# Kernel tuning notes

Hardware: AMD Instinct MI355X
Metric: run time of the kernel (lower is better)

Reference implementation:

```python
import jax, jax.numpy as jnp
import numpy as np

ALPHA = 0.2   # LeakyReLU negative slope
NEG = -1e9    # mask value for non-edges


def setup_inputs() -> dict:
    key = jax.random.key(0)
    ks = jax.random.split(key, 8)
    N, Din, F, H, Dout = 4096, 512, 64, 8, 16
    adj = (jax.random.uniform(ks[0], (N, N)) < 0.01).astype(jnp.float32)
    adjacency = jnp.maximum(adj, jnp.eye(N, dtype=jnp.float32))
    X = jax.random.normal(ks[1], (N, Din), jnp.float32)
    s = lambda k, shape, fan: jax.random.normal(k, shape, jnp.float32) / np.float32(np.sqrt(fan))
    W = s(ks[2], (H, Din, F), Din)        # per-head projection, stacked
    a1 = s(ks[3], (H, F), F)              # attention vector, source half
    a2 = s(ks[4], (H, F), F)              # attention vector, target half
    Wo = s(ks[5], (H * F, Dout), H * F)   # output-layer projection
    ao1 = s(ks[6], (Dout,), Dout)
    ao2 = s(ks[7], (Dout,), Dout)
    return dict(adjacency=adjacency, X=X, W=W, a1=a1, a2=a2, Wo=Wo, ao1=ao1, ao2=ao2)


def reference(adjacency, X, W, a1, a2, Wo, ao1, ao2):
    # dropout is identity (eval mode / p=0)
    mask = adjacency > 0
    N = X.shape[0]
    # --- multi-head attention layers (concat=True -> ELU) ---
    Wh = jnp.einsum('nd,hdf->hnf', X, W)                      # [H, N, F]
    f1 = jnp.einsum('hnf,hf->hn', Wh, a1)                     # [H, N]
    f2 = jnp.einsum('hnf,hf->hn', Wh, a2)                     # [H, N]
    e = jax.nn.leaky_relu(f1[:, :, None] + f2[:, None, :], ALPHA)  # [H, N, N]
    att = jax.nn.softmax(jnp.where(mask[None], e, NEG), axis=-1)
    heads = jax.nn.elu(jnp.einsum('hnm,hmf->hnf', att, Wh))   # [H, N, F]
    cat = jnp.transpose(heads, (1, 0, 2)).reshape(N, -1)      # [N, H*F]
    # --- output attention layer (concat=False -> no ELU) ---
    Who = cat @ Wo                                            # [N, Dout]
    eo = jax.nn.leaky_relu((Who @ ao1)[:, None] + (Who @ ao2)[None, :], ALPHA)
    atto = jax.nn.softmax(jnp.where(mask, eo, NEG), axis=-1)  # [N, N]
    return atto @ Who                                         # [N, Dout]
```

## Files before the change

### kernel.cpp

```cpp
#include <hip/hip_runtime.h>
#include <hip/hip_bf16.h>

#define N_NODES 4096
#define DIN     512
#define FDIM    64
#define NHEADS  8
#define DOUT    16
#define MAXN    512

typedef __attribute__((ext_vector_type(8))) short bf16x8;
typedef __attribute__((ext_vector_type(4))) float f32x4;

static __device__ __forceinline__ float us2f(unsigned short u) {
    union { unsigned int i; float f; } cv; cv.i = ((unsigned int)u) << 16; return cv.f;
}
static __device__ __forceinline__ unsigned short f2us(float v) {
    __hip_bfloat16 b = __float2bfloat16(v);
    return *(const unsigned short*)&b;
}

__global__ void detect_kernel(const unsigned short* __restrict__ adj, int* __restrict__ flag)
{
    if (threadIdx.x == 0) *flag = (adj[0] == 0) ? 1 : 0;
}

__global__ __launch_bounds__(256) void build_nbr_kernel(
    const void* __restrict__ adj, const int* __restrict__ flag,
    int* __restrict__ cnt, int* __restrict__ nbr)
{
    const int n = blockIdx.x;
    const int f32 = *flag;
    __shared__ int c;
    if (threadIdx.x == 0) c = 0;
    __syncthreads();
    if (f32) {
        const unsigned int* row = (const unsigned int*)adj + (size_t)n * N_NODES;
        for (int m = threadIdx.x; m < N_NODES; m += 256) {
            if (row[m]) { int p = atomicAdd(&c, 1); if (p < MAXN) nbr[(size_t)n * MAXN + p] = m; }
        }
    } else {
        const unsigned short* row = (const unsigned short*)adj + (size_t)n * N_NODES;
        for (int m = threadIdx.x; m < N_NODES; m += 256) {
            if (row[m]) { int p = atomicAdd(&c, 1); if (p < MAXN) nbr[(size_t)n * MAXN + p] = m; }
        }
    }
    __syncthreads();
    if (threadIdx.x == 0) cnt[n] = (c < MAXN) ? c : MAXN;
}

__global__ __launch_bounds__(256) void conv_small_kernel(
    const void* __restrict__ a1, const void* __restrict__ a2, const void* __restrict__ Wo,
    const void* __restrict__ ao1, const void* __restrict__ ao2,
    const int* __restrict__ flag, float* __restrict__ dst)
{
    const int f32 = *flag;
    const void* srcs[5] = { a1, a2, Wo, ao1, ao2 };
    const int   szs[5]  = { 512, 512, 8192, 16, 16 };
    int base = 0;
    for (int s = 0; s < 5; ++s) {
        if (f32) {
            for (int i = threadIdx.x; i < szs[s]; i += 256)
                dst[base + i] = ((const float*)srcs[s])[i];
        } else {
            for (int i = threadIdx.x; i < szs[s]; i += 256)
                dst[base + i] = us2f(((const unsigned short*)srcs[s])[i]);
        }
        base += szs[s];
    }
}

__global__ __launch_bounds__(256) void wh_mfma_kernel(
    const void* __restrict__ X, const void* __restrict__ W,
    const int* __restrict__ flag, unsigned short* __restrict__ Whb)
{
    __shared__ unsigned short Ah[64][72];
    __shared__ unsigned short Al[64][72];
    __shared__ unsigned short Bt[64][72];
    const int f32 = *flag;
    const int h  = blockIdx.x;
    const int bm = blockIdx.y;
    const int tid  = threadIdx.x;
    const int w    = tid >> 6;
    const int lane = tid & 63;
    const int quad = lane >> 4;
    const int l16  = lane & 15;
    const int r  = tid >> 2;
    const int c4 = (tid & 3) * 16;

    f32x4 acc[4];
#pragma unroll
    for (int j = 0; j < 4; ++j) acc[j] = (f32x4){0.f, 0.f, 0.f, 0.f};

    for (int k0 = 0; k0 < DIN; k0 += 64) {
        if (f32) {
            const float* xp = (const float*)X + (size_t)(bm * 64 + r) * DIN + k0 + c4;
            const float* wp = (const float*)W + (size_t)h * DIN * FDIM + (size_t)(k0 + r) * FDIM + c4;
#pragma unroll
            for (int i = 0; i < 16; ++i) {
                float v = xp[i];
                unsigned short hi = f2us(v);
                Ah[r][c4 + i] = hi;
                Al[r][c4 + i] = f2us(v - us2f(hi));
            }
#pragma unroll
            for (int i = 0; i < 16; ++i) Bt[c4 + i][r] = f2us(wp[i]);
        } else {
            const unsigned short* xp = (const unsigned short*)X + (size_t)(bm * 64 + r) * DIN + k0 + c4;
            const unsigned short* wp = (const unsigned short*)W + (size_t)h * DIN * FDIM + (size_t)(k0 + r) * FDIM + c4;
#pragma unroll
            for (int i = 0; i < 16; ++i) { Ah[r][c4 + i] = xp[i]; Al[r][c4 + i] = 0; }
#pragma unroll
            for (int i = 0; i < 16; ++i) Bt[c4 + i][r] = wp[i];
        }
        __syncthreads();
#pragma unroll
        for (int kk = 0; kk < 64; kk += 32) {
            bf16x8 a_hi = *(const bf16x8*)&Ah[w * 16 + l16][kk + quad * 8];
            bf16x8 a_lo = *(const bf16x8*)&Al[w * 16 + l16][kk + quad * 8];
#pragma unroll
            for (int j = 0; j < 4; ++j) {
                bf16x8 b = *(const bf16x8*)&Bt[j * 16 + l16][kk + quad * 8];
                acc[j] = __builtin_amdgcn_mfma_f32_16x16x32_bf16(a_hi, b, acc[j], 0, 0, 0);
                acc[j] = __builtin_amdgcn_mfma_f32_16x16x32_bf16(a_lo, b, acc[j], 0, 0, 0);
            }
        }
        __syncthreads();
    }
#pragma unroll
    for (int j = 0; j < 4; ++j) {
        int col = j * 16 + l16;
#pragma unroll
        for (int rr = 0; rr < 4; ++rr) {
            int row = bm * 64 + w * 16 + quad * 4 + rr;
            Whb[((size_t)h * N_NODES + row) * FDIM + col] = f2us(acc[j][rr]);
        }
    }
}

__global__ __launch_bounds__(256) void f12_kernel(
    const unsigned short* __restrict__ Whb,
    const float* __restrict__ a1c, const float* __restrict__ a2c,
    float* __restrict__ f1, float* __restrict__ f2)
{
    int idx = blockIdx.x * 256 + threadIdx.x;
    int h = idx >> 12;
    const unsigned short* row = Whb + (size_t)idx * FDIM;
    float s1 = 0.f, s2 = 0.f;
#pragma unroll
    for (int f = 0; f < FDIM; ++f) {
        float v = us2f(row[f]);
        s1 += v * a1c[h * FDIM + f];
        s2 += v * a2c[h * FDIM + f];
    }
    f1[idx] = s1;
    f2[idx] = s2;
}

__global__ __launch_bounds__(256) void attn1_kernel(
    const unsigned short* __restrict__ Whb,
    const float* __restrict__ f1, const float* __restrict__ f2,
    const int* __restrict__ cnt, const int* __restrict__ nbr,
    unsigned short* __restrict__ catb)
{
    const int n = blockIdx.x;
    const int tid = threadIdx.x;
    const int wid = tid >> 6;
    const int lane = tid & 63;
    __shared__ int sh_m[MAXN];
    __shared__ float sh_s[4][MAXN];
    const int c0 = cnt[n];
    const int c = (c0 < MAXN) ? c0 : MAXN;
    for (int k = tid; k < c; k += 256) sh_m[k] = nbr[(size_t)n * MAXN + k];
    __syncthreads();
    for (int hh = 0; hh < 2; ++hh) {
        const int h = wid * 2 + hh;
        const float f1v = f1[h * N_NODES + n];
        float mx = -1e30f;
        for (int k = lane; k < c; k += 64) {
            float s = f1v + f2[h * N_NODES + sh_m[k]];
            s = (s >= 0.f) ? s : 0.2f * s;
            sh_s[wid][k] = s;
            mx = fmaxf(mx, s);
        }
#pragma unroll
        for (int off = 32; off; off >>= 1) mx = fmaxf(mx, __shfl_xor(mx, off));
        float sum = 0.f;
        for (int k = lane; k < c; k += 64) {
            float e = __expf(sh_s[wid][k] - mx);
            sh_s[wid][k] = e;
            sum += e;
        }
#pragma unroll
        for (int off = 32; off; off >>= 1) sum += __shfl_xor(sum, off);
        const float inv = (sum > 0.f) ? 1.f / sum : 0.f;
        float acc = 0.f;
        for (int k = 0; k < c; ++k)
            acc += sh_s[wid][k] * us2f(Whb[((size_t)h * N_NODES + sh_m[k]) * FDIM + lane]);
        acc *= inv;
        acc = (acc > 0.f) ? acc : expm1f(acc);
        catb[(size_t)n * (NHEADS * FDIM) + h * FDIM + lane] = f2us(acc);
        __syncthreads();
    }
}

__global__ __launch_bounds__(256) void who_kernel(
    const unsigned short* __restrict__ catb, const float* __restrict__ Woc,
    float* __restrict__ Who)
{
    __shared__ float sWo[DIN * DOUT];
    for (int l = threadIdx.x; l < DIN * DOUT; l += 256) sWo[l] = Woc[l];
    __syncthreads();
    const int i = threadIdx.x >> 4;
    const int j = threadIdx.x & 15;
    const int n = blockIdx.x * 16 + i;
    const unsigned short* crow = catb + (size_t)n * DIN;
    float acc = 0.f;
    for (int d = 0; d < DIN; ++d) acc += us2f(crow[d]) * sWo[d * DOUT + j];
    Who[n * DOUT + j] = acc;
}

__global__ __launch_bounds__(256) void g12_kernel(
    const float* __restrict__ Who,
    const float* __restrict__ ao1c, const float* __restrict__ ao2c,
    float* __restrict__ g1, float* __restrict__ g2)
{
    int n = blockIdx.x * 256 + threadIdx.x;
    float s1 = 0.f, s2 = 0.f;
#pragma unroll
    for (int j = 0; j < DOUT; ++j) {
        float v = Who[n * DOUT + j];
        s1 += v * ao1c[j];
        s2 += v * ao2c[j];
    }
    g1[n] = s1;
    g2[n] = s2;
}

__global__ __launch_bounds__(64) void attn2_kernel(
    const float* __restrict__ Who,
    const float* __restrict__ g1, const float* __restrict__ g2,
    const int* __restrict__ cnt, const int* __restrict__ nbr,
    const int* __restrict__ flag, void* __restrict__ out)
{
    const int n = blockIdx.x;
    const int lane = threadIdx.x;
    __shared__ float sh_s[MAXN];
    __shared__ int sh_m[MAXN];
    const int c0 = cnt[n];
    const int c = (c0 < MAXN) ? c0 : MAXN;
    for (int k = lane; k < c; k += 64) sh_m[k] = nbr[(size_t)n * MAXN + k];
    __syncthreads();
    const float gn = g1[n];
    float mx = -1e30f;
    for (int k = lane; k < c; k += 64) {
        float s = gn + g2[sh_m[k]];
        s = (s >= 0.f) ? s : 0.2f * s;
        sh_s[k] = s;
        mx = fmaxf(mx, s);
    }
#pragma unroll
    for (int off = 32; off; off >>= 1) mx = fmaxf(mx, __shfl_xor(mx, off));
    __syncthreads();
    float sum = 0.f;
    for (int k = lane; k < c; k += 64) {
        float e = __expf(sh_s[k] - mx);
        sh_s[k] = e;
        sum += e;
    }
#pragma unroll
    for (int off = 32; off; off >>= 1) sum += __shfl_xor(sum, off);
    __syncthreads();
    const float inv = (sum > 0.f) ? 1.f / sum : 0.f;
    if (lane < DOUT) {
        float acc = 0.f;
        for (int k = 0; k < c; ++k) acc += sh_s[k] * Who[sh_m[k] * DOUT + lane];
        acc *= inv;
        if (*flag) ((float*)out)[n * DOUT + lane] = acc;
        else       ((unsigned short*)out)[n * DOUT + lane] = f2us(acc);
    }
}

__global__ void wsfail_kernel(float* __restrict__ out)
{
    if (threadIdx.x == 0) out[0] = 129.f;
}

extern "C" void kernel_launch(void* const* d_in, const int* in_sizes, int n_in,
                              void* d_out, int out_size, void* d_ws, size_t ws_size,
                              hipStream_t stream)
{
    const void* adj = d_in[0];
    const void* X   = d_in[1];
    const void* W   = d_in[2];
    const void* a1  = d_in[3];
    const void* a2  = d_in[4];
    const void* Wo  = d_in[5];
    const void* ao1 = d_in[6];
    const void* ao2 = d_in[7];

    const size_t NEEDED = 17400000;
    if (ws_size < NEEDED) { wsfail_kernel<<<1, 64, 0, stream>>>((float*)d_out); return; }

    int* flag = (int*)d_ws;
    int* cnt  = flag + 1;
    int* nbr  = cnt + 4096;
    float* smalls = (float*)(nbr + 2097152);
    float* a1c  = smalls;
    float* a2c  = smalls + 512;
    float* Woc  = smalls + 1024;
    float* ao1c = smalls + 9216;
    float* ao2c = smalls + 9232;
    float* f1   = smalls + 9248;
    float* f2   = f1 + 32768;
    float* Who  = f2 + 32768;
    float* g1   = Who + 65536;
    float* g2   = g1 + 4096;
    unsigned short* Whb  = (unsigned short*)(g2 + 4096);
    unsigned short* catb = Whb + 2097152;

    detect_kernel<<<1, 64, 0, stream>>>((const unsigned short*)adj, flag);
    build_nbr_kernel<<<N_NODES, 256, 0, stream>>>(adj, flag, cnt, nbr);
    conv_small_kernel<<<1, 256, 0, stream>>>(a1, a2, Wo, ao1, ao2, flag, smalls);
    wh_mfma_kernel<<<dim3(NHEADS, N_NODES / 64), 256, 0, stream>>>(X, W, flag, Whb);
    f12_kernel<<<128, 256, 0, stream>>>(Whb, a1c, a2c, f1, f2);
    attn1_kernel<<<N_NODES, 256, 0, stream>>>(Whb, f1, f2, cnt, nbr, catb);
    who_kernel<<<N_NODES / 16, 256, 0, stream>>>(catb, Woc, Who);
    g12_kernel<<<N_NODES / 256, 256, 0, stream>>>(Who, ao1c, ao2c, g1, g2);
    attn2_kernel<<<N_NODES, 64, 0, stream>>>(Who, g1, g2, cnt, nbr, flag, d_out);
}
```

Baseline: 198.4 us.

## Merge setup kernels, vectorize loads, use MFMA for output projection with fused g12

Merges flag detection and small-weight conversion into one setup kernel, which also writes a transposed hi/lo bf16 split of Wo. The output projection moves from scalar shared-memory FMA to MFMA over that split, with the g1/g2 dot products folded into its epilogue via shuffles, so the g12 kernel goes away. Adjacency scanning, X/W staging and f12 loads are vectorized, and f12 is relaunched with 128-thread blocks. attn2 now spreads the neighbor aggregation over all 64 lanes instead of 16. Together these cut kernel launches and serial scalar work.

```diff
diff --git a/kernel.cpp b/kernel.cpp
--- a/kernel.cpp
+++ b/kernel.cpp
@@ -19,41 +19,21 @@
     return *(const unsigned short*)&b;
 }
 
-__global__ void detect_kernel(const unsigned short* __restrict__ adj, int* __restrict__ flag)
-{
-    if (threadIdx.x == 0) *flag = (adj[0] == 0) ? 1 : 0;
-}
-
-__global__ __launch_bounds__(256) void build_nbr_kernel(
-    const void* __restrict__ adj, const int* __restrict__ flag,
-    int* __restrict__ cnt, int* __restrict__ nbr)
-{
-    const int n = blockIdx.x;
-    const int f32 = *flag;
-    __shared__ int c;
-    if (threadIdx.x == 0) c = 0;
-    __syncthreads();
-    if (f32) {
-        const unsigned int* row = (const unsigned int*)adj + (size_t)n * N_NODES;
-        for (int m = threadIdx.x; m < N_NODES; m += 256) {
-            if (row[m]) { int p = atomicAdd(&c, 1); if (p < MAXN) nbr[(size_t)n * MAXN + p] = m; }
-        }
-    } else {
-        const unsigned short* row = (const unsigned short*)adj + (size_t)n * N_NODES;
-        for (int m = threadIdx.x; m < N_NODES; m += 256) {
-            if (row[m]) { int p = atomicAdd(&c, 1); if (p < MAXN) nbr[(size_t)n * MAXN + p] = m; }
-        }
-    }
-    __syncthreads();
-    if (threadIdx.x == 0) cnt[n] = (c < MAXN) ? c : MAXN;
-}
-
-__global__ __launch_bounds__(256) void conv_small_kernel(
+__global__ __launch_bounds__(256) void setup_kernel(
+    const void* __restrict__ adjv,
     const void* __restrict__ a1, const void* __restrict__ a2, const void* __restrict__ Wo,
     const void* __restrict__ ao1, const void* __restrict__ ao2,
-    const int* __restrict__ flag, float* __restrict__ dst)
-{
-    const int f32 = *flag;
+    int* __restrict__ flag, float* __restrict__ dst,
+    unsigned short* __restrict__ WtH, unsigned short* __restrict__ WtL)
+{
+    __shared__ int sflag;
+    if (threadIdx.x == 0) {
+        int f = (((const unsigned short*)adjv)[0] == 0) ? 1 : 0;
+        *flag = f;
+        sflag = f;
+    }
+    __syncthreads();
+    const int f32 = sflag;
     const void* srcs[5] = { a1, a2, Wo, ao1, ao2 };
     const int   szs[5]  = { 512, 512, 8192, 16, 16 };
     int base = 0;
@@ -67,6 +47,49 @@
         }
         base += szs[s];
     }
+    __syncthreads();
+    const float* Woc = dst + 1024;
+    for (int l = threadIdx.x; l < DIN * DOUT; l += 256) {
+        int d = l >> 4, j = l & 15;
+        float v = Woc[l];
+        unsigned short hi = f2us(v);
+        WtH[j * DIN + d] = hi;
+        WtL[j * DIN + d] = f2us(v - us2f(hi));
+    }
+}
+
+__global__ __launch_bounds__(256) void build_nbr_kernel(
+    const void* __restrict__ adj, const int* __restrict__ flag,
+    int* __restrict__ cnt, int* __restrict__ nbr)
+{
+    const int n = blockIdx.x;
+    const int f32 = *flag;
+    __shared__ int c;
+    if (threadIdx.x == 0) c = 0;
+    __syncthreads();
+    if (f32) {
+        const uint4* row = (const uint4*)((const unsigned int*)adj + (size_t)n * N_NODES);
+        for (int q = threadIdx.x; q < N_NODES / 4; q += 256) {
+            uint4 v = row[q];
+            int base = q * 4;
+            if (v.x) { int p = atomicAdd(&c, 1); if (p < MAXN) nbr[(size_t)n * MAXN + p] = base + 0; }
+            if (v.y) { int p = atomicAdd(&c, 1); if (p < MAXN) nbr[(size_t)n * MAXN + p] = base + 1; }
+            if (v.z) { int p = atomicAdd(&c, 1); if (p < MAXN) nbr[(size_t)n * MAXN + p] = base + 2; }
+            if (v.w) { int p = atomicAdd(&c, 1); if (p < MAXN) nbr[(size_t)n * MAXN + p] = base + 3; }
+        }
+    } else {
+        const ushort4* row = (const ushort4*)((const unsigned short*)adj + (size_t)n * N_NODES);
+        for (int q = threadIdx.x; q < N_NODES / 4; q += 256) {
+            ushort4 v = row[q];
+            int base = q * 4;
+            if (v.x) { int p = atomicAdd(&c, 1); if (p < MAXN) nbr[(size_t)n * MAXN + p] = base + 0; }
+            if (v.y) { int p = atomicAdd(&c, 1); if (p < MAXN) nbr[(size_t)n * MAXN + p] = base + 1; }
+            if (v.z) { int p = atomicAdd(&c, 1); if (p < MAXN) nbr[(size_t)n * MAXN + p] = base + 2; }
+            if (v.w) { int p = atomicAdd(&c, 1); if (p < MAXN) nbr[(size_t)n * MAXN + p] = base + 3; }
+        }
+    }
+    __syncthreads();
+    if (threadIdx.x == 0) cnt[n] = (c < MAXN) ? c : MAXN;
 }
 
 __global__ __launch_bounds__(256) void wh_mfma_kernel(
@@ -96,14 +119,25 @@
             const float* xp = (const float*)X + (size_t)(bm * 64 + r) * DIN + k0 + c4;
             const float* wp = (const float*)W + (size_t)h * DIN * FDIM + (size_t)(k0 + r) * FDIM + c4;
 #pragma unroll
-            for (int i = 0; i < 16; ++i) {
-                float v = xp[i];
-                unsigned short hi = f2us(v);
-                Ah[r][c4 + i] = hi;
-                Al[r][c4 + i] = f2us(v - us2f(hi));
+            for (int i4 = 0; i4 < 4; ++i4) {
+                float4 v4 = ((const float4*)xp)[i4];
+                float vv[4] = { v4.x, v4.y, v4.z, v4.w };
+#pragma unroll
+                for (int t = 0; t < 4; ++t) {
+                    int i = i4 * 4 + t;
+                    unsigned short hi = f2us(vv[t]);
+                    Ah[r][c4 + i] = hi;
+                    Al[r][c4 + i] = f2us(vv[t] - us2f(hi));
+                }
             }
 #pragma unroll
-            for (int i = 0; i < 16; ++i) Bt[c4 + i][r] = f2us(wp[i]);
+            for (int i4 = 0; i4 < 4; ++i4) {
+                float4 v4 = ((const float4*)wp)[i4];
+                Bt[c4 + i4 * 4 + 0][r] = f2us(v4.x);
+                Bt[c4 + i4 * 4 + 1][r] = f2us(v4.y);
+                Bt[c4 + i4 * 4 + 2][r] = f2us(v4.z);
+                Bt[c4 + i4 * 4 + 3][r] = f2us(v4.w);
+            }
         } else {
             const unsigned short* xp = (const unsigned short*)X + (size_t)(bm * 64 + r) * DIN + k0 + c4;
             const unsigned short* wp = (const unsigned short*)W + (size_t)h * DIN * FDIM + (size_t)(k0 + r) * FDIM + c4;
@@ -137,20 +171,25 @@
     }
 }
 
-__global__ __launch_bounds__(256) void f12_kernel(
+__global__ __launch_bounds__(128) void f12_kernel(
     const unsigned short* __restrict__ Whb,
     const float* __restrict__ a1c, const float* __restrict__ a2c,
     float* __restrict__ f1, float* __restrict__ f2)
 {
-    int idx = blockIdx.x * 256 + threadIdx.x;
+    int idx = blockIdx.x * 128 + threadIdx.x;
     int h = idx >> 12;
-    const unsigned short* row = Whb + (size_t)idx * FDIM;
+    const bf16x8* row = (const bf16x8*)(Whb + (size_t)idx * FDIM);
     float s1 = 0.f, s2 = 0.f;
 #pragma unroll
-    for (int f = 0; f < FDIM; ++f) {
-        float v = us2f(row[f]);
-        s1 += v * a1c[h * FDIM + f];
-        s2 += v * a2c[h * FDIM + f];
+    for (int q = 0; q < 8; ++q) {
+        bf16x8 v8 = row[q];
+#pragma unroll
+        for (int t = 0; t < 8; ++t) {
+            float v = us2f((unsigned short)v8[t]);
+            int f = q * 8 + t;
+            s1 += v * a1c[h * FDIM + f];
+            s2 += v * a2c[h * FDIM + f];
+        }
     }
     f1[idx] = s1;
     f2[idx] = s2;
@@ -203,37 +242,37 @@
     }
 }
 
-__global__ __launch_bounds__(256) void who_kernel(
-    const unsigned short* __restrict__ catb, const float* __restrict__ Woc,
-    float* __restrict__ Who)
-{
-    __shared__ float sWo[DIN * DOUT];
-    for (int l = threadIdx.x; l < DIN * DOUT; l += 256) sWo[l] = Woc[l];
-    __syncthreads();
-    const int i = threadIdx.x >> 4;
-    const int j = threadIdx.x & 15;
-    const int n = blockIdx.x * 16 + i;
-    const unsigned short* crow = catb + (size_t)n * DIN;
-    float acc = 0.f;
-    for (int d = 0; d < DIN; ++d) acc += us2f(crow[d]) * sWo[d * DOUT + j];
-    Who[n * DOUT + j] = acc;
-}
-
-__global__ __launch_bounds__(256) void g12_kernel(
-    const float* __restrict__ Who,
+__global__ __launch_bounds__(64) void who_mfma_g_kernel(
+    const unsigned short* __restrict__ catb,
+    const unsigned short* __restrict__ WtH, const unsigned short* __restrict__ WtL,
     const float* __restrict__ ao1c, const float* __restrict__ ao2c,
-    float* __restrict__ g1, float* __restrict__ g2)
-{
-    int n = blockIdx.x * 256 + threadIdx.x;
-    float s1 = 0.f, s2 = 0.f;
-#pragma unroll
-    for (int j = 0; j < DOUT; ++j) {
-        float v = Who[n * DOUT + j];
-        s1 += v * ao1c[j];
-        s2 += v * ao2c[j];
-    }
-    g1[n] = s1;
-    g2[n] = s2;
+    float* __restrict__ Who, float* __restrict__ g1, float* __restrict__ g2)
+{
+    const int lane = threadIdx.x;
+    const int quad = lane >> 4, l16 = lane & 15;
+    const int row0 = blockIdx.x * 16;
+    f32x4 acc = (f32x4){0.f, 0.f, 0.f, 0.f};
+    for (int k0 = 0; k0 < DIN; k0 += 32) {
+        bf16x8 a  = *(const bf16x8*)&catb[(size_t)(row0 + l16) * DIN + k0 + quad * 8];
+        bf16x8 bh = *(const bf16x8*)&WtH[l16 * DIN + k0 + quad * 8];
+        bf16x8 bl = *(const bf16x8*)&WtL[l16 * DIN + k0 + quad * 8];
+        acc = __builtin_amdgcn_mfma_f32_16x16x32_bf16(a, bh, acc, 0, 0, 0);
+        acc = __builtin_amdgcn_mfma_f32_16x16x32_bf16(a, bl, acc, 0, 0, 0);
+    }
+#pragma unroll
+    for (int rr = 0; rr < 4; ++rr) {
+        int row = row0 + quad * 4 + rr;
+        float v = acc[rr];
+        Who[row * DOUT + l16] = v;
+        float p1 = v * ao1c[l16];
+        float p2 = v * ao2c[l16];
+#pragma unroll
+        for (int off = 8; off; off >>= 1) {
+            p1 += __shfl_xor(p1, off);
+            p2 += __shfl_xor(p2, off);
+        }
+        if (l16 == 0) { g1[row] = p1; g2[row] = p2; }
+    }
 }
 
 __global__ __launch_bounds__(64) void attn2_kernel(
@@ -244,6 +283,7 @@
 {
     const int n = blockIdx.x;
     const int lane = threadIdx.x;
+    const int quad = lane >> 4, l16 = lane & 15;
     __shared__ float sh_s[MAXN];
     __shared__ int sh_m[MAXN];
     const int c0 = cnt[n];
@@ -271,12 +311,15 @@
     for (int off = 32; off; off >>= 1) sum += __shfl_xor(sum, off);
     __syncthreads();
     const float inv = (sum > 0.f) ? 1.f / sum : 0.f;
-    if (lane < DOUT) {
-        float acc = 0.f;
-        for (int k = 0; k < c; ++k) acc += sh_s[k] * Who[sh_m[k] * DOUT + lane];
-        acc *= inv;
-        if (*flag) ((float*)out)[n * DOUT + lane] = acc;
-        else       ((unsigned short*)out)[n * DOUT + lane] = f2us(acc);
+    float accv = 0.f;
+    for (int k = quad; k < c; k += 4)
+        accv += sh_s[k] * Who[sh_m[k] * DOUT + l16];
+    accv += __shfl_xor(accv, 16);
+    accv += __shfl_xor(accv, 32);
+    if (quad == 0) {
+        float v = accv * inv;
+        if (*flag) ((float*)out)[n * DOUT + l16] = v;
+        else       ((unsigned short*)out)[n * DOUT + l16] = f2us(v);
     }
 }
 
@@ -298,7 +341,7 @@
     const void* ao1 = d_in[6];
     const void* ao2 = d_in[7];
 
-    const size_t NEEDED = 17400000;
+    const size_t NEEDED = 17500000;
     if (ws_size < NEEDED) { wsfail_kernel<<<1, 64, 0, stream>>>((float*)d_out); return; }
 
     int* flag = (int*)d_ws;
@@ -307,7 +350,6 @@
     float* smalls = (float*)(nbr + 2097152);
     float* a1c  = smalls;
     float* a2c  = smalls + 512;
-    float* Woc  = smalls + 1024;
     float* ao1c = smalls + 9216;
     float* ao2c = smalls + 9232;
     float* f1   = smalls + 9248;
@@ -317,14 +359,14 @@
     float* g2   = g1 + 4096;
     unsigned short* Whb  = (unsigned short*)(g2 + 4096);
     unsigned short* catb = Whb + 2097152;
-
-    detect_kernel<<<1, 64, 0, stream>>>((const unsigned short*)adj, flag);
+    unsigned short* WtH  = catb + 2097152;
+    unsigned short* WtL  = WtH + 8192;
+
+    setup_kernel<<<1, 256, 0, stream>>>(adj, a1, a2, Wo, ao1, ao2, flag, smalls, WtH, WtL);
     build_nbr_kernel<<<N_NODES, 256, 0, stream>>>(adj, flag, cnt, nbr);
-    conv_small_kernel<<<1, 256, 0, stream>>>(a1, a2, Wo, ao1, ao2, flag, smalls);
     wh_mfma_kernel<<<dim3(NHEADS, N_NODES / 64), 256, 0, stream>>>(X, W, flag, Whb);
-    f12_kernel<<<128, 256, 0, stream>>>(Whb, a1c, a2c, f1, f2);
+    f12_kernel<<<256, 128, 0, stream>>>(Whb, a1c, a2c, f1, f2);
     attn1_kernel<<<N_NODES, 256, 0, stream>>>(Whb, f1, f2, cnt, nbr, catb);
-    who_kernel<<<N_NODES / 16, 256, 0, stream>>>(catb, Woc, Who);
-    g12_kernel<<<N_NODES / 256, 256, 0, stream>>>(Who, ao1c, ao2c, g1, g2);
+    who_mfma_g_kernel<<<N_NODES / 16, 64, 0, stream>>>(catb, WtH, WtL, ao1c, ao2c, Who, g1, g2);
     attn2_kernel<<<N_NODES, 64, 0, stream>>>(Who, g1, g2, cnt, nbr, flag, d_out);
 }
```

New measurement: 183.7 us. -7.4%, faster.
